# Optimization experiments

Hardware: AMD Instinct MI355X
Metric: run time of the kernel (lower is better)

## Reference

```python
import jax, jax.numpy as jnp
import numpy as np

N, NC, D, K = 262144, 4096, 5, 4   # fine dof, coarse dof, nnz/row of A, interp points/row of P
W = 2.0 / 3.0                      # weighted-Jacobi weight
PRE, POST, COARSE = 3, 3, 10       # smoothing counts from the source


def setup_inputs() -> dict:
    key = jax.random.key(0)
    k1, k2, k3, k4, k5 = jax.random.split(key, 5)
    # A in ELL form: slot 0 is the diagonal, made strictly diagonally dominant.
    acols_off = jax.random.randint(k1, (N, D - 1), 0, N)
    A_cols = jnp.concatenate([jnp.arange(N)[:, None], acols_off], axis=1).astype(jnp.int32)
    off = -jax.random.uniform(k2, (N, D - 1), dtype=jnp.float32)          # negative off-diagonals (M-matrix-like)
    diag = 2.0 + jnp.sum(jnp.abs(off), axis=1)
    A_vals = jnp.concatenate([diag[:, None], off], axis=1)
    # P in ELL form: slot 0 maps fine node i -> coarse node i // (N//NC) so every coarse dof is covered.
    pcols_off = jax.random.randint(k3, (N, K - 1), 0, NC)
    P_cols = jnp.concatenate([(jnp.arange(N) // (N // NC))[:, None], pcols_off], axis=1).astype(jnp.int32)
    P_vals = jax.random.uniform(k4, (N, K), dtype=jnp.float32) * 0.5
    b = jax.random.normal(k5, (N,), dtype=jnp.float32)
    x = jnp.zeros((N,), dtype=jnp.float32)
    return {"b": b, "x": x, "A_vals": A_vals, "P_vals": P_vals,
            "A_cols": A_cols, "P_cols": P_cols, "num": 2}


def _spmv(vals, cols, x):
    # ELL SpMV: y[i] = sum_d vals[i,d] * x[cols[i,d]]
    return jnp.sum(vals * x[cols], axis=1)


def _jacobi_ell(vals, cols, diag, b, x, n):
    def step(xc, _):
        return xc + W * (b - _spmv(vals, cols, xc)) / diag, None
    x, _ = jax.lax.scan(step, x, None, length=n)
    return x


def _rap(A_vals, A_cols, P_vals, P_cols):
    # A_c = P^T A P, assembled densely on the coarse level via one big scatter-add.
    Pj_vals = P_vals[A_cols]                                   # [N,D,K]
    Pj_cols = P_cols[A_cols]                                   # [N,D,K]
    vals = (P_vals[:, None, :, None] * A_vals[:, :, None, None]
            * Pj_vals[:, :, None, :])                          # [N,D,K,K]
    a_idx = jnp.broadcast_to(P_cols[:, None, :, None].astype(jnp.int32), (N, D, K, K))
    b_idx = jnp.broadcast_to(Pj_cols[:, :, None, :].astype(jnp.int32), (N, D, K, K))
    flat = (a_idx * NC + b_idx).reshape(-1)
    Ac = jax.ops.segment_sum(vals.reshape(-1), flat, num_segments=NC * NC)
    return Ac.reshape(NC, NC)


def reference(b, x, A_vals, P_vals, A_cols, P_cols, num):
    diag_f = A_vals[:, 0]                      # fine-level diagonal (slot 0)
    Ac = _rap(A_vals, A_cols, P_vals, P_cols)  # coarse operator R A P
    diag_c = jnp.diag(Ac)

    def coarse_solve(bc):
        def step(xc, _):
            return xc + W * (bc - Ac @ xc) / diag_c, None
        xc, _ = jax.lax.scan(step, jnp.zeros((NC,), bc.dtype), None, length=COARSE)
        return xc

    for _ in range(num):                       # mg.Iterate, `num` V-cycles
        x = _jacobi_ell(A_vals, A_cols, diag_f, b, x, PRE)          # pre-smooth
        r = b - _spmv(A_vals, A_cols, x)                            # residual
        bc = jax.ops.segment_sum((P_vals * r[:, None]).reshape(-1),  # restrict: R r = P^T r
                                 P_cols.reshape(-1), num_segments=NC)
        xc = coarse_solve(bc)                                       # coarse Jacobi solve
        x = x + jnp.sum(P_vals * xc[P_cols], axis=1)                # prolongate correction
        x = _jacobi_ell(A_vals, A_cols, diag_f, b, x, POST)         # post-smooth
    return x
```

## Files before the change

kernel.cpp:

```cpp
#include <hip/hip_runtime.h>
#include <hip/hip_fp16.h>

#define NN 262144
#define NCC 4096
#define DD 5
#define PRE_IT 3
#define POST_IT 3
#define COARSE_IT 10
#define WJ ((float)(2.0/3.0))
#define NBLK 256
#define BAR_SLOT_U32 768
#define BAR_SLOTS 40
#define POISON 0xAAAAAAAAu
#define BASE_SUM 0x55555540u

typedef unsigned long long u64;

__device__ __forceinline__ unsigned pack_ch(unsigned col, float v) {
  return col | ((unsigned)__half_as_ushort(__float2half(v)) << 16);
}
__device__ __forceinline__ float unpack_h(unsigned w) {
  return __half2float(__ushort_as_half((unsigned short)(w >> 16)));
}

__device__ __forceinline__ float ldA(const float* p) {
  return __hip_atomic_load(p, __ATOMIC_RELAXED, __HIP_MEMORY_SCOPE_AGENT);
}
__device__ __forceinline__ void stA(float* p, float v) {
  __hip_atomic_store(p, v, __ATOMIC_RELAXED, __HIP_MEMORY_SCOPE_AGENT);
}
__device__ __forceinline__ unsigned ldAu(const unsigned* p) {
  return __hip_atomic_load(p, __ATOMIC_RELAXED, __HIP_MEMORY_SCOPE_AGENT);
}
__device__ __forceinline__ void stAu(unsigned* p, unsigned v) {
  __hip_atomic_store(p, v, __ATOMIC_RELAXED, __HIP_MEMORY_SCOPE_AGENT);
}
__device__ __forceinline__ u64 ldA64(const u64* p) {
  return __hip_atomic_load(p, __ATOMIC_RELAXED, __HIP_MEMORY_SCOPE_AGENT);
}
__device__ __forceinline__ void stA64(u64* p, u64 v) {
  __hip_atomic_store(p, v, __ATOMIC_RELAXED, __HIP_MEMORY_SCOPE_AGENT);
}

__device__ __forceinline__ void gbar(unsigned* bar, int& bs, int* sflag) {
  __syncthreads();
  if (threadIdx.x == 0) {
    unsigned* slot  = bar + bs * BAR_SLOT_U32;
    unsigned* line  = slot + ((blockIdx.x & 31) << 4);
    unsigned* flags = slot + 512;
    unsigned r = __hip_atomic_fetch_add(line, 1u, __ATOMIC_RELAXED,
                                        __HIP_MEMORY_SCOPE_AGENT);
    if ((blockIdx.x & 31) == 0 && r == POISON + 7u) {
      for (;;) {
        unsigned s = 0;
#pragma unroll
        for (int i = 0; i < 32; ++i) s += ldAu(slot + (i << 4));
        if (s - BASE_SUM >= 256u) break;
        __builtin_amdgcn_s_sleep(1);
      }
#pragma unroll
      for (int f = 0; f < 16; ++f) stAu(flags + (f << 4), POISON + 1u);
    }
    const unsigned* fl = flags + ((blockIdx.x & 15) << 4);
    while (ldAu(fl) == POISON) __builtin_amdgcn_s_sleep(1);
    __hip_atomic_store(sflag, bs + 1, __ATOMIC_RELAXED, __HIP_MEMORY_SCOPE_WORKGROUP);
  } else if ((threadIdx.x & 63) == 0) {
    while (__hip_atomic_load(sflag, __ATOMIC_RELAXED, __HIP_MEMORY_SCOPE_WORKGROUP) <= bs)
      __builtin_amdgcn_s_sleep(1);
  }
  ++bs;
}

__global__ __launch_bounds__(1024, 4) void k_all(
    const float* __restrict__ b, const float* __restrict__ x_in,
    const float* __restrict__ A_vals, const float* __restrict__ P_vals,
    const int* __restrict__ A_cols, const int* __restrict__ P_cols,
    const int* __restrict__ num_p,
    unsigned* histG, unsigned* offsG, u64* pairs8,
    unsigned* Y, unsigned* tot,
    unsigned* bar, float* partials, float* x2,
    float* xcA, float* xcB, float* out) {
  extern __shared__ char smem[];
  __shared__ float wdiag[16];
  __shared__ float bcl[16];
  __shared__ unsigned soffs[17];
  __shared__ int sflag;

  const int tid = threadIdx.x;
  const int blk = blockIdx.x;
  const int g = (blk << 10) + tid;
  int bs = 0;
  if (tid == 0) sflag = 0;

  const int4* pc4 = (const int4*)P_cols;
  const float4* pv4 = (const float4*)P_vals;
  unsigned* base_t = histG;

  {
    unsigned* s1 = (unsigned*)smem;
    unsigned* s2 = s1 + NCC;
    unsigned* s3 = s2 + NCC;
    unsigned* sv = s3 + NCC;

    const int4 pc = pc4[g];
    const float4 pv = pv4[g];

    for (int q = tid; q < NCC; q += 1024) s1[q] = 0u;
    __syncthreads();
    {
      int ac[DD]; float av[DD];
#pragma unroll
      for (int j = 0; j < DD; ++j) { ac[j] = A_cols[g * DD + j]; av[j] = A_vals[g * DD + j]; }
      u64* yp = (u64*)(Y + 20u * (unsigned)g);
#pragma unroll
      for (int j = 0; j < DD; ++j) {
        const int4 pcn = pc4[ac[j]];
        const float4 pvn = pv4[ac[j]];
        const u64 lo = (u64)pack_ch((unsigned)pcn.x, av[j] * pvn.x)
                     | ((u64)pack_ch((unsigned)pcn.y, av[j] * pvn.y) << 32);
        const u64 hi = (u64)pack_ch((unsigned)pcn.z, av[j] * pvn.z)
                     | ((u64)pack_ch((unsigned)pcn.w, av[j] * pvn.w) << 32);
        stA64(yp + 2 * j, lo);
        stA64(yp + 2 * j + 1, hi);
      }
    }
    atomicAdd(&s1[pc.x], 1u); atomicAdd(&s1[pc.y], 1u);
    atomicAdd(&s1[pc.z], 1u); atomicAdd(&s1[pc.w], 1u);
    __syncthreads();
    for (int q = tid; q < NCC; q += 1024) stAu(&histG[(blk << 12) + q], s1[q]);
    gbar(bar, bs, &sflag);

    {
      const int w = tid >> 6, l = tid & 63;
      const int c = (blk << 4) + w;
      const unsigned h0 = ldAu(&histG[(((l << 2) + 0) << 12) + c]);
      const unsigned h1 = ldAu(&histG[(((l << 2) + 1) << 12) + c]);
      const unsigned h2 = ldAu(&histG[(((l << 2) + 2) << 12) + c]);
      const unsigned h3 = ldAu(&histG[(((l << 2) + 3) << 12) + c]);
      const unsigned s = h0 + h1 + h2 + h3;
      unsigned scan = s;
#pragma unroll
      for (int d = 1; d < 64; d <<= 1) {
        unsigned v = __shfl_up(scan, d);
        if (l >= d) scan += v;
      }
      const unsigned pre = scan - s;
      stAu(&base_t[(((l << 2) + 0) << 12) + c], pre);
      stAu(&base_t[(((l << 2) + 1) << 12) + c], pre + h0);
      stAu(&base_t[(((l << 2) + 2) << 12) + c], pre + h0 + h1);
      stAu(&base_t[(((l << 2) + 3) << 12) + c], pre + h0 + h1 + h2);
      if (l == 63) stAu(&tot[c], scan);
    }
    gbar(bar, bs, &sflag);

    {
      for (int q = tid; q < NCC; q += 1024) s1[q] = ldAu(&tot[q]);
      __syncthreads();
      const unsigned a0 = s1[(tid << 2) + 0], a1 = s1[(tid << 2) + 1],
                     a2 = s1[(tid << 2) + 2], a3 = s1[(tid << 2) + 3];
      const unsigned tsum = a0 + a1 + a2 + a3;
      sv[tid] = tsum; __syncthreads();
      for (int off = 1; off < 1024; off <<= 1) {
        unsigned v = (tid >= off) ? sv[tid - off] : 0u;
        __syncthreads();
        sv[tid] += v;
        __syncthreads();
      }
      const unsigned excl = sv[tid] - tsum;
      s1[(tid << 2) + 0] = excl;
      s1[(tid << 2) + 1] = excl + a0;
      s1[(tid << 2) + 2] = excl + a0 + a1;
      s1[(tid << 2) + 3] = excl + a0 + a1 + a2;
      __syncthreads();
      if (tid < 16) stAu(&offsG[(blk << 4) + tid], s1[(blk << 4) + tid]);
      if (blk == 255 && tid == 1023) stAu(&offsG[NCC], excl + tsum);
      for (int q = tid; q < NCC; q += 1024)
        s2[q] = s1[q] + ldAu(&base_t[(blk << 12) + q]);
      for (int q = tid; q < NCC; q += 1024) s3[q] = 0u;
      __syncthreads();
      unsigned r;
      r = atomicAdd(&s3[pc.x], 1u);
      stA64(&pairs8[s2[pc.x] + r], (u64)(unsigned)g | ((u64)__float_as_uint(pv.x) << 32));
      r = atomicAdd(&s3[pc.y], 1u);
      stA64(&pairs8[s2[pc.y] + r], (u64)(unsigned)g | ((u64)__float_as_uint(pv.y) << 32));
      r = atomicAdd(&s3[pc.z], 1u);
      stA64(&pairs8[s2[pc.z] + r], (u64)(unsigned)g | ((u64)__float_as_uint(pv.z) << 32));
      r = atomicAdd(&s3[pc.w], 1u);
      stA64(&pairs8[s2[pc.w] + r], (u64)(unsigned)g | ((u64)__float_as_uint(pv.w) << 32));
    }
    gbar(bar, bs, &sflag);
  }

  __half* slab   = (__half*)smem;
  float* rowbuf  = (float*)(smem + 131072);
  float* rowbuf1 = (float*)(smem + 114688);

  if (tid < 17) soffs[tid] = ldAu(&offsG[(blk << 4) + tid]);

#define SCAT(rb, yk) { \
    const unsigned lo_ = (unsigned)(yk), hi_ = (unsigned)((yk) >> 32); \
    atomicAdd(&rb[lo_ & 0xffffu], pvf * unpack_h(lo_)); \
    atomicAdd(&rb[hi_ & 0xffffu], pvf * unpack_h(hi_)); }

  for (int rp = 0; rp < 8; ++rp) {
    if (rp < 7) {
      const int r0 = rp << 1, r1 = r0 + 1;
      for (int q = tid; q < NCC; q += 1024) { rowbuf[q] = 0.f; rowbuf1[q] = 0.f; }
      __syncthreads();
      const unsigned q0 = soffs[r0], q1 = soffs[r1], q2 = soffs[r1 + 1];
      for (unsigned p = q0 + tid; p < q2; p += 1024) {
        float* rb = (p < q1) ? rowbuf : rowbuf1;
        const u64 e = ldA64(&pairs8[p]);
        const float pvf = __uint_as_float((unsigned)(e >> 32));
        const u64* yp = (const u64*)(Y + 20u * (unsigned)(e & 0xffffffffu));
        u64 y0 = ldA64(yp + 0), y1 = ldA64(yp + 1), y2 = ldA64(yp + 2), y3 = ldA64(yp + 3),
            y4 = ldA64(yp + 4), y5 = ldA64(yp + 5), y6 = ldA64(yp + 6), y7 = ldA64(yp + 7),
            y8 = ldA64(yp + 8), y9 = ldA64(yp + 9);
        SCAT(rb, y0) SCAT(rb, y1) SCAT(rb, y2) SCAT(rb, y3) SCAT(rb, y4)
        SCAT(rb, y5) SCAT(rb, y6) SCAT(rb, y7) SCAT(rb, y8) SCAT(rb, y9)
      }
      __syncthreads();
      if (tid == 0) {
        wdiag[r0] = WJ / rowbuf[(blk << 4) + r0];
        wdiag[r1] = WJ / rowbuf1[(blk << 4) + r1];
      }
      for (int q = tid; q < NCC; q += 1024) {
        slab[(r0 << 12) + q] = __float2half(rowbuf[q]);
        slab[(r1 << 12) + q] = __float2half(rowbuf1[q]);
      }
      __syncthreads();
    } else {
      for (int rr = 14; rr < 16; ++rr) {
        const int c1 = (blk << 4) + rr;
        for (int q = tid; q < NCC; q += 1024) rowbuf[q] = 0.f;
        __syncthreads();
        const unsigned p0 = soffs[rr], p1 = soffs[rr + 1];
        for (unsigned p = p0 + tid; p < p1; p += 1024) {
          const u64 e = ldA64(&pairs8[p]);
          const float pvf = __uint_as_float((unsigned)(e >> 32));
          const u64* yp = (const u64*)(Y + 20u * (unsigned)(e & 0xffffffffu));
          u64 y0 = ldA64(yp + 0), y1 = ldA64(yp + 1), y2 = ldA64(yp + 2), y3 = ldA64(yp + 3),
              y4 = ldA64(yp + 4), y5 = ldA64(yp + 5), y6 = ldA64(yp + 6), y7 = ldA64(yp + 7),
              y8 = ldA64(yp + 8), y9 = ldA64(yp + 9);
          SCAT(rowbuf, y0) SCAT(rowbuf, y1) SCAT(rowbuf, y2) SCAT(rowbuf, y3) SCAT(rowbuf, y4)
          SCAT(rowbuf, y5) SCAT(rowbuf, y6) SCAT(rowbuf, y7) SCAT(rowbuf, y8) SCAT(rowbuf, y9)
        }
        __syncthreads();
        if (tid == 0) wdiag[rr] = WJ / rowbuf[c1];
        for (int q = tid; q < NCC; q += 1024) slab[(rr << 12) + q] = __float2half(rowbuf[q]);
        __syncthreads();
      }
    }
  }
#undef SCAT

  const int num = num_p[0];
  if (num <= 0) { stA(out + g, x_in[g]); return; }

  float av[DD]; int ac[DD];
#pragma unroll
  for (int j = 0; j < DD; ++j) { av[j] = A_vals[g * DD + j]; ac[j] = A_cols[g * DD + j]; }
  const float bg = b[g];
  const float wdg = WJ / av[0];
  const int4 pcg = pc4[g];
  const float4 pvg = pv4[g];
  float xown = x_in[g];

  const float* xr = x_in;
  int wi = 0;

  for (int cyc = 0; cyc < num; ++cyc) {
    for (int it = 0; it < PRE_IT; ++it) {
      float s = av[0] * xown;
#pragma unroll
      for (int j = 1; j < DD; ++j) s += av[j] * ldA(xr + ac[j]);
      const float xn = xown + (bg - s) * wdg;
      float* wb = (wi == 0) ? x2 : out;
      stA(wb + g, xn);
      xown = xn; xr = wb; wi ^= 1;
      gbar(bar, bs, &sflag);
    }
    {
      float s = av[0] * xown;
#pragma unroll
      for (int j = 1; j < DD; ++j) s += av[j] * ldA(xr + ac[j]);
      const float r = bg - s;
      for (int q = tid; q < NCC; q += 1024) rowbuf[q] = 0.f;
      __syncthreads();
      atomicAdd(&rowbuf[pcg.x], pvg.x * r);
      atomicAdd(&rowbuf[pcg.y], pvg.y * r);
      atomicAdd(&rowbuf[pcg.z], pvg.z * r);
      atomicAdd(&rowbuf[pcg.w], pvg.w * r);
      __syncthreads();
      for (int q = tid; q < NCC; q += 1024) stA(&partials[(blk << 12) + q], rowbuf[q]);
      gbar(bar, bs, &sflag);
    }
    {
      const int t2 = tid >> 2;
      const u64* pp = (const u64*)&partials[(t2 << 12) + (blk << 4)];
      const int qq = (tid & 3) << 1;
      const u64 va = ldA64(pp + qq);
      const u64 vb = ldA64(pp + qq + 1);
      ((u64*)rowbuf)[(t2 << 3) + qq] = va;
      ((u64*)rowbuf)[(t2 << 3) + qq + 1] = vb;
      __syncthreads();
      if (tid < 16) {
        float sum = 0.f;
#pragma unroll 8
        for (int t3 = 0; t3 < 256; ++t3) sum += rowbuf[(t3 << 4) + tid];
        bcl[tid] = sum;
        stA(&xcA[(blk << 4) + tid], sum * wdiag[tid]);
      }
      gbar(bar, bs, &sflag);
    }
    const float* xc_cur = xcA;
    float* xc_nxt = xcB;
    for (int it = 1; it < COARSE_IT; ++it) {
      const int w = tid >> 6, l = tid & 63;
      const int xb = (w << 8) + (l << 2);
      const u64* xp = (const u64*)(xc_cur + xb);
      const u64 xlo = ldA64(xp), xhi = ldA64(xp + 1);
      float4 xv;
      xv.x = __uint_as_float((unsigned)xlo); xv.y = __uint_as_float((unsigned)(xlo >> 32));
      xv.z = __uint_as_float((unsigned)xhi); xv.w = __uint_as_float((unsigned)(xhi >> 32));
      float acc[16];
#pragma unroll
      for (int r2 = 0; r2 < 16; ++r2) {
        const __half2* hp2 = (const __half2*)(slab + (r2 << 12) + (w << 8) + (l << 2));
        const float2 f01 = __half22float2(hp2[0]);
        const float2 f23 = __half22float2(hp2[1]);
        acc[r2] = f01.x * xv.x + f01.y * xv.y + f23.x * xv.z + f23.y * xv.w;
      }
#pragma unroll
      for (int r2 = 0; r2 < 16; ++r2) {
        float v = acc[r2];
        v += __shfl_down(v, 32); v += __shfl_down(v, 16); v += __shfl_down(v, 8);
        v += __shfl_down(v, 4);  v += __shfl_down(v, 2);  v += __shfl_down(v, 1);
        acc[r2] = v;
      }
      if (l == 0) {
#pragma unroll
        for (int r2 = 0; r2 < 16; ++r2) rowbuf[(w << 4) + r2] = acc[r2];
      }
      __syncthreads();
      if (tid < 16) {
        float y = 0.f;
#pragma unroll
        for (int w2 = 0; w2 < 16; ++w2) y += rowbuf[(w2 << 4) + tid];
        const float xo = ldA(xc_cur + (blk << 4) + tid);
        stA(&xc_nxt[(blk << 4) + tid], xo + (bcl[tid] - y) * wdiag[tid]);
      }
      float* tmp = (float*)xc_cur; xc_cur = xc_nxt; xc_nxt = tmp;
      gbar(bar, bs, &sflag);
    }
    {
      const u64* xq = (const u64*)(xc_cur + (tid << 2));
      const u64 qa = ldA64(xq), qb = ldA64(xq + 1);
      ((u64*)rowbuf)[(tid << 1)] = qa;
      ((u64*)rowbuf)[(tid << 1) + 1] = qb;
      __syncthreads();
      float* xw = (float*)xr;
      const float corr = pvg.x * rowbuf[pcg.x] + pvg.y * rowbuf[pcg.y] +
                         pvg.z * rowbuf[pcg.z] + pvg.w * rowbuf[pcg.w];
      const float xn = xown + corr;
      stA(xw + g, xn);
      xown = xn;
      gbar(bar, bs, &sflag);
    }
    for (int it = 0; it < POST_IT; ++it) {
      float s = av[0] * xown;
#pragma unroll
      for (int j = 1; j < DD; ++j) s += av[j] * ldA(xr + ac[j]);
      const float xn = xown + (bg - s) * wdg;
      float* wb = (wi == 0) ? x2 : out;
      stA(wb + g, xn);
      xown = xn; xr = wb; wi ^= 1;
      if (!(cyc == num - 1 && it == POST_IT - 1)) gbar(bar, bs, &sflag);
    }
  }
}

extern "C" void kernel_launch(void* const* d_in, const int* in_sizes, int n_in,
                              void* d_out, int out_size, void* d_ws, size_t ws_size,
                              hipStream_t stream) {
  (void)in_sizes; (void)n_in; (void)out_size; (void)ws_size;
  const float* b      = (const float*)d_in[0];
  const float* x_in   = (const float*)d_in[1];
  const float* A_vals = (const float*)d_in[2];
  const float* P_vals = (const float*)d_in[3];
  const int*   A_cols = (const int*)d_in[4];
  const int*   P_cols = (const int*)d_in[5];
  const int*   num_p  = (const int*)d_in[6];
  float* out = (float*)d_out;

  char* ws = (char*)d_ws;
  unsigned* offsG  = (unsigned*)(ws + 0);
  unsigned* tot    = (unsigned*)(ws + 20480);
  float*    xcA    = (float*)(ws + 40960);
  float*    xcB    = (float*)(ws + 57344);
  unsigned* bar    = (unsigned*)(ws + 73728);
  u64*      pairs8 = (u64*)(ws + 262144);
  unsigned* histG  = (unsigned*)(ws + 8650752);
  unsigned* Y      = (unsigned*)(ws + 12845056);
  float* partials  = (float*)Y;
  float* x2        = (float*)histG;


  const unsigned smem_bytes = 131072 + 16384;
  hipFuncSetAttribute((const void*)k_all,
                      hipFuncAttributeMaxDynamicSharedMemorySize, (int)smem_bytes);
  hipLaunchKernelGGL(k_all, dim3(NBLK), dim3(1024), smem_bytes, stream,
                     b, x_in, A_vals, P_vals, A_cols, P_cols, num_p,
                     histG, offsG, pairs8, Y, tot,
                     bar, partials, x2, xcA, xcB, out);
}
```

Baseline: 544.4 us.

## Assign one coarse row per wavefront in coarse Jacobi matvec with LDS-staged x

The coarse Jacobi iteration now stages the whole coarse vector in shared memory each iteration, and each wavefront computes one full row of the block's 16 coarse rows. Previously each wavefront took a 256-column slice of all 16 rows and needed 16 shuffle reductions plus a cross-wave shared-memory reduction. The new mapping cuts the reduction to one shuffle chain and removes one sync stage. It also uses 16-byte slab loads, at the cost of a full-vector LDS load per iteration. This assumes the slab layout puts each row's 4096 halfs contiguously at w<<12, which must match how the slab was written.

```diff
diff --git a/kernel.cpp b/kernel.cpp
--- a/kernel.cpp
+++ b/kernel.cpp
@@ -316,39 +316,33 @@
     const float* xc_cur = xcA;
     float* xc_nxt = xcB;
     for (int it = 1; it < COARSE_IT; ++it) {
+      const u64* xq = (const u64*)(xc_cur + (tid << 2));
+      const u64 qa = ldA64(xq), qb = ldA64(xq + 1);
+      ((u64*)rowbuf)[(tid << 1)] = qa;
+      ((u64*)rowbuf)[(tid << 1) + 1] = qb;
+      __syncthreads();
       const int w = tid >> 6, l = tid & 63;
-      const int xb = (w << 8) + (l << 2);
-      const u64* xp = (const u64*)(xc_cur + xb);
-      const u64 xlo = ldA64(xp), xhi = ldA64(xp + 1);
-      float4 xv;
-      xv.x = __uint_as_float((unsigned)xlo); xv.y = __uint_as_float((unsigned)(xlo >> 32));
-      xv.z = __uint_as_float((unsigned)xhi); xv.w = __uint_as_float((unsigned)(xhi >> 32));
-      float acc[16];
-#pragma unroll
-      for (int r2 = 0; r2 < 16; ++r2) {
-        const __half2* hp2 = (const __half2*)(slab + (r2 << 12) + (w << 8) + (l << 2));
-        const float2 f01 = __half22float2(hp2[0]);
-        const float2 f23 = __half22float2(hp2[1]);
-        acc[r2] = f01.x * xv.x + f01.y * xv.y + f23.x * xv.z + f23.y * xv.w;
-      }
-#pragma unroll
-      for (int r2 = 0; r2 < 16; ++r2) {
-        float v = acc[r2];
-        v += __shfl_down(v, 32); v += __shfl_down(v, 16); v += __shfl_down(v, 8);
-        v += __shfl_down(v, 4);  v += __shfl_down(v, 2);  v += __shfl_down(v, 1);
-        acc[r2] = v;
-      }
+      const __half* srow = slab + (w << 12);
+      float acc = 0.f;
+#pragma unroll
+      for (int k = 0; k < 8; ++k) {
+        const int cb = (k << 9) + (l << 3);
+        const uint4 hv = *(const uint4*)(srow + cb);
+        const float4 x0 = *(const float4*)(rowbuf + cb);
+        const float4 x1 = *(const float4*)(rowbuf + cb + 4);
+        const float2 h0 = __half22float2(__builtin_bit_cast(__half2, hv.x));
+        const float2 h1 = __half22float2(__builtin_bit_cast(__half2, hv.y));
+        const float2 h2 = __half22float2(__builtin_bit_cast(__half2, hv.z));
+        const float2 h3 = __half22float2(__builtin_bit_cast(__half2, hv.w));
+        acc += h0.x * x0.x + h0.y * x0.y + h1.x * x0.z + h1.y * x0.w;
+        acc += h2.x * x1.x + h2.y * x1.y + h3.x * x1.z + h3.y * x1.w;
+      }
+      acc += __shfl_down(acc, 32); acc += __shfl_down(acc, 16);
+      acc += __shfl_down(acc, 8);  acc += __shfl_down(acc, 4);
+      acc += __shfl_down(acc, 2);  acc += __shfl_down(acc, 1);
       if (l == 0) {
-#pragma unroll
-        for (int r2 = 0; r2 < 16; ++r2) rowbuf[(w << 4) + r2] = acc[r2];
-      }
-      __syncthreads();
-      if (tid < 16) {
-        float y = 0.f;
-#pragma unroll
-        for (int w2 = 0; w2 < 16; ++w2) y += rowbuf[(w2 << 4) + tid];
-        const float xo = ldA(xc_cur + (blk << 4) + tid);
-        stA(&xc_nxt[(blk << 4) + tid], xo + (bcl[tid] - y) * wdiag[tid]);
+        const float xo = rowbuf[(blk << 4) + w];
+        stA(&xc_nxt[(blk << 4) + w], xo + (bcl[w] - acc) * wdiag[w]);
       }
       float* tmp = (float*)xc_cur; xc_cur = xc_nxt; xc_nxt = tmp;
       gbar(bar, bs, &sflag);
```

Measured after the change: 487.2 us. 10.5% less time.
